# Optimization experiments

Measured on AMD Instinct MI355X. Metric: run time of the kernel, lower is better.

## Reference

```python
import jax, jax.numpy as jnp
import numpy as np

EPS = 1e-7  # K.epsilon()


def setup_inputs() -> dict:
    key = jax.random.key(0)
    k1, k2, k3 = jax.random.split(key, 3)
    B, T, D = 32, 2048, 1024
    one = jax.random.normal(k1, (B, D), dtype=jnp.float32)
    many = jax.random.normal(k2, (B, T, D), dtype=jnp.float32)
    W = jax.random.normal(k3, (D, D), dtype=jnp.float32) * (1.0 / np.sqrt(D))
    return {"one": one, "many": many, "W": W}


def reference(one, many, W):
    # logits = batch_dot(tanh(many @ W), one, axes=[2,1]) -> [B, T]
    proj = jnp.tanh(jnp.einsum('btd,de->bte', many, W))       # [B,T,D]
    logits = jnp.einsum('btd,bd->bt', proj, one)               # [B,T]
    # stable softmax with Keras epsilon in denominator
    ai = jnp.exp(logits - jnp.max(logits, axis=-1, keepdims=True))
    att_weights = ai / (jnp.sum(ai, axis=-1, keepdims=True) + EPS)  # [B,T]
    result = jnp.einsum('btd,bt->bd', many, att_weights)       # [B,D]
    return result, att_weights
```

## Files before the change

### kernel.cpp

```cpp
#include <hip/hip_runtime.h>
#include <hip/hip_bf16.h>

typedef _Float16 half8v __attribute__((ext_vector_type(8)));
typedef __fp16  fp16x2 __attribute__((ext_vector_type(2)));
typedef float floatx4 __attribute__((ext_vector_type(4)));

#define NB 32
#define NT 2048
#define ND 1024
#define NM (NB * NT)

#define GL16(g, l)                                                             \
    __builtin_amdgcn_global_load_lds(                                          \
        (const __attribute__((address_space(1))) void*)(g),                    \
        (__attribute__((address_space(3))) void*)(l), 16, 0, 0)

__device__ __forceinline__ float fast_tanh(float x) {
    x = fminf(9.0f, fmaxf(-9.0f, x));
    float e = __builtin_amdgcn_exp2f(x * 2.8853900817779268f);
    return (e - 1.0f) * __builtin_amdgcn_rcpf(e + 1.0f);
}

__global__ __launch_bounds__(256)
void wt_kernel(const float* __restrict__ W, _Float16* __restrict__ Wt) {
    __shared__ float tile[32][33];
    int tx = threadIdx.x, ty = threadIdx.y;
    int bx = blockIdx.x, by = blockIdx.y;
    #pragma unroll
    for (int i = 0; i < 4; ++i) {
        int y = by * 32 + ty + i * 8;
        tile[ty + i * 8][tx] = W[y * ND + bx * 32 + tx];
    }
    __syncthreads();
    #pragma unroll
    for (int i = 0; i < 4; ++i) {
        int e = bx * 32 + ty + i * 8;
        Wt[e * ND + by * 32 + tx] = (_Float16)tile[tx][ty + i * 8];
    }
}

__global__ __launch_bounds__(256, 2)
void gemm_logits(const float* __restrict__ many, const _Float16* __restrict__ Wt,
                 const float* __restrict__ one, float* __restrict__ logits) {
    __shared__ uint4 AsQ[2048];
    __shared__ uint4 BsQ[1024];
    char* AsB = (char*)AsQ;
    char* BsB = (char*)BsQ;

    int bid = blockIdx.x;
    int j = (bid & 7) * 512 + (bid >> 3);
    int mb = j >> 3, nb = j & 7;
    int m0 = mb * 128, n0 = nb * 128;

    int tid = threadIdx.x;
    int lane = tid & 63, w = tid >> 6;
    int wr = w >> 1, wc = w & 1;
    int l15 = lane & 15, l4 = lane >> 4;

    const char* aS = (const char*)many
        + ((size_t)(m0 + (tid >> 4)) << 12)
        + (size_t)(((tid & 15) ^ ((tid >> 4) & 7)) << 4);
    const char* bS = (const char*)Wt
        + ((size_t)(n0 + (tid >> 3)) << 11)
        + (size_t)(((tid & 7) ^ ((tid >> 3) & 7)) << 4);
    char* aD = AsB + tid * 16;
    char* bD = BsB + tid * 16;

    floatx4 acc[4][4] = {};

    for (int kb = 0; kb < 1024; kb += 64) {
        #pragma unroll
        for (int i = 0; i < 8; ++i)
            GL16(aS + kb * 4 + i * 65536, aD + i * 4096);
        #pragma unroll
        for (int i = 0; i < 4; ++i)
            GL16(bS + kb * 2 + i * 65536, bD + i * 4096);
        __syncthreads();

        #pragma unroll
        for (int ks = 0; ks < 64; ks += 32) {
            half8v af[4], bf[4];
            #pragma unroll
            for (int mi = 0; mi < 4; ++mi) {
                int r = wr * 64 + mi * 16 + l15;
                int s = l15 & 7;
                const char* base = AsB + r * 256;
                int c0 = (ks >> 2) + l4 * 2;
                float4 x = *(const float4*)(base + (size_t)((c0 ^ s) << 4));
                float4 y = *(const float4*)(base + (size_t)(((c0 + 1) ^ s) << 4));
                union { fp16x2 p[4]; half8v h; } u;
                u.p[0] = __builtin_amdgcn_cvt_pkrtz(x.x, x.y);
                u.p[1] = __builtin_amdgcn_cvt_pkrtz(x.z, x.w);
                u.p[2] = __builtin_amdgcn_cvt_pkrtz(y.x, y.y);
                u.p[3] = __builtin_amdgcn_cvt_pkrtz(y.z, y.w);
                af[mi] = u.h;
            }
            #pragma unroll
            for (int ni = 0; ni < 4; ++ni) {
                int r = wc * 64 + ni * 16 + l15;
                int s = l15 & 7;
                int c = (ks >> 3) + l4;
                bf[ni] = *(const half8v*)(BsB + r * 128 + (size_t)((c ^ s) << 4));
            }
            #pragma unroll
            for (int mi = 0; mi < 4; ++mi)
                #pragma unroll
                for (int ni = 0; ni < 4; ++ni)
                    acc[mi][ni] = __builtin_amdgcn_mfma_f32_16x16x32_f16(
                        af[mi], bf[ni], acc[mi][ni], 0, 0, 0);
        }
        __syncthreads();
    }

    int bidx = m0 >> 11;
    float onev[4];
    #pragma unroll
    for (int ni = 0; ni < 4; ++ni)
        onev[ni] = one[(bidx << 10) + n0 + wc * 64 + ni * 16 + l15];

    #pragma unroll
    for (int mi = 0; mi < 4; ++mi) {
        float part[4] = {0.f, 0.f, 0.f, 0.f};
        #pragma unroll
        for (int ni = 0; ni < 4; ++ni)
            #pragma unroll
            for (int b = 0; b < 4; ++b)
                part[b] += fast_tanh(acc[mi][ni][b]) * onev[ni];
        #pragma unroll
        for (int off = 1; off < 16; off <<= 1)
            #pragma unroll
            for (int b = 0; b < 4; ++b)
                part[b] += __shfl_xor(part[b], off, 64);
        #pragma unroll
        for (int b = 0; b < 4; ++b)
            if (l15 == mi * 4 + b)
                atomicAdd(&logits[m0 + wr * 64 + mi * 16 + l4 * 4 + b], part[b]);
    }
}

__global__ __launch_bounds__(256)
void softmax_kernel(const float* __restrict__ logits, float* __restrict__ att) {
    int b = blockIdx.x, tid = threadIdx.x;
    const float* lr = logits + (b << 11);
    float lv[8];
    float mx = -1e30f;
    #pragma unroll
    for (int i = 0; i < 8; ++i) { lv[i] = lr[tid + (i << 8)]; mx = fmaxf(mx, lv[i]); }
    #pragma unroll
    for (int off = 1; off < 64; off <<= 1) mx = fmaxf(mx, __shfl_xor(mx, off, 64));
    __shared__ float redm[4];
    __shared__ float reds[4];
    int wv = tid >> 6;
    if ((tid & 63) == 0) redm[wv] = mx;
    __syncthreads();
    mx = fmaxf(fmaxf(redm[0], redm[1]), fmaxf(redm[2], redm[3]));
    float s = 0.f;
    #pragma unroll
    for (int i = 0; i < 8; ++i) { lv[i] = expf(lv[i] - mx); s += lv[i]; }
    #pragma unroll
    for (int off = 1; off < 64; off <<= 1) s += __shfl_xor(s, off, 64);
    if ((tid & 63) == 0) reds[wv] = s;
    __syncthreads();
    s = reds[0] + reds[1] + reds[2] + reds[3];
    float inv = 1.0f / (s + 1e-7f);
    #pragma unroll
    for (int i = 0; i < 8; ++i) att[(b << 11) + tid + (i << 8)] = lv[i] * inv;
}

__global__ __launch_bounds__(256)
void out_kernel(const float* __restrict__ many, const float* __restrict__ att,
                float* __restrict__ out) {
    int b = blockIdx.x >> 4, tch = blockIdx.x & 15;
    int tid = threadIdx.x;
    __shared__ float aw[128];
    if (tid < 128) aw[tid] = att[(b << 11) + tch * 128 + tid];
    __syncthreads();
    const float* mp = many + (((size_t)b * NT + tch * 128) << 10) + tid * 4;
    float ax = 0.f, ay = 0.f, az = 0.f, aww = 0.f;
    for (int t = 0; t < 128; ++t) {
        float wgt = aw[t];
        float4 v = *reinterpret_cast<const float4*>(mp + ((size_t)t << 10));
        ax = fmaf(v.x, wgt, ax); ay = fmaf(v.y, wgt, ay);
        az = fmaf(v.z, wgt, az); aww = fmaf(v.w, wgt, aww);
    }
    float* op = out + (b << 10) + tid * 4;
    atomicAdd(op + 0, ax); atomicAdd(op + 1, ay);
    atomicAdd(op + 2, az); atomicAdd(op + 3, aww);
}

extern "C" void kernel_launch(void* const* d_in, const int* in_sizes, int n_in,
                              void* d_out, int out_size, void* d_ws, size_t ws_size,
                              hipStream_t stream) {
    const float* one  = (const float*)d_in[0];
    const float* many = (const float*)d_in[1];
    const float* W    = (const float*)d_in[2];
    float* out = (float*)d_out;

    _Float16* Wt  = (_Float16*)d_ws;
    float* logits = (float*)((char*)d_ws + (size_t)ND * ND * 2);
    float* att    = out + NB * ND;

    (void)hipMemsetAsync(out, 0, (size_t)NB * ND * sizeof(float), stream);
    (void)hipMemsetAsync(logits, 0, (size_t)NM * sizeof(float), stream);

    wt_kernel<<<dim3(32, 32), dim3(32, 8), 0, stream>>>(W, Wt);
    gemm_logits<<<4096, 256, 0, stream>>>(many, Wt, one, logits);
    softmax_kernel<<<NB, 256, 0, stream>>>(logits, att);
    out_kernel<<<NB * 16, 256, 0, stream>>>(many, att, out);
}
```

Measured before the change: 242.9 us.

## Pre-convert many to fp16 and double-buffer the GEMM LDS pipeline

After: 260.5 us. +7.2%, slower.

```diff
diff --git a/kernel.cpp b/kernel.cpp
--- a/kernel.cpp
+++ b/kernel.cpp
@@ -36,6 +36,123 @@
     for (int i = 0; i < 4; ++i) {
         int e = bx * 32 + ty + i * 8;
         Wt[e * ND + by * 32 + tx] = (_Float16)tile[tx][ty + i * 8];
+    }
+}
+
+__global__ __launch_bounds__(256)
+void conv_kernel(const float* __restrict__ many, _Float16* __restrict__ manyh) {
+    size_t idx = ((size_t)blockIdx.x * 256 + threadIdx.x) * 8;
+    size_t stride = (size_t)gridDim.x * 256 * 8;
+    for (size_t i = idx; i < (size_t)NM * ND; i += stride) {
+        float4 a = *reinterpret_cast<const float4*>(many + i);
+        float4 b = *reinterpret_cast<const float4*>(many + i + 4);
+        union { _Float16 h[8]; uint4 u; } o;
+        o.h[0] = (_Float16)a.x; o.h[1] = (_Float16)a.y;
+        o.h[2] = (_Float16)a.z; o.h[3] = (_Float16)a.w;
+        o.h[4] = (_Float16)b.x; o.h[5] = (_Float16)b.y;
+        o.h[6] = (_Float16)b.z; o.h[7] = (_Float16)b.w;
+        *reinterpret_cast<uint4*>(manyh + i) = o.u;
+    }
+}
+
+__global__ __launch_bounds__(256, 2)
+void gemm_logits_h(const _Float16* __restrict__ manyh, const _Float16* __restrict__ Wt,
+                   const float* __restrict__ one, float* __restrict__ logits) {
+    __shared__ uint4 LDSQ[4096];
+    char* Ld = (char*)LDSQ;
+
+    int bid = blockIdx.x;
+    int j = (bid & 7) * 512 + (bid >> 3);
+    int mb = j >> 3, nb = j & 7;
+    int m0 = mb * 128, n0 = nb * 128;
+
+    int tid = threadIdx.x;
+    int lane = tid & 63, w = tid >> 6;
+    int wr = w >> 1, wc = w & 1;
+    int l15 = lane & 15, l4 = lane >> 4;
+
+    const char* aS = (const char*)manyh + ((size_t)(m0 + (tid >> 3)) << 11)
+                   + (size_t)(((tid & 7) ^ ((tid >> 3) & 7)) << 4);
+    const char* bS = (const char*)Wt + ((size_t)(n0 + (tid >> 3)) << 11)
+                   + (size_t)(((tid & 7) ^ ((tid >> 3) & 7)) << 4);
+
+    floatx4 acc[4][4] = {};
+
+#define STAGE(KB, BUFOFF) do {                                                 \
+    int kby_ = (KB) * 2;                                                       \
+    _Pragma("unroll")                                                          \
+    for (int i_ = 0; i_ < 4; ++i_)                                             \
+        GL16(aS + kby_ + i_ * 65536, Ld + (BUFOFF) + tid * 16 + i_ * 4096);    \
+    _Pragma("unroll")                                                          \
+    for (int i_ = 0; i_ < 4; ++i_)                                             \
+        GL16(bS + kby_ + i_ * 65536,                                           \
+             Ld + (BUFOFF) + 16384 + tid * 16 + i_ * 4096);                    \
+} while (0)
+
+#define COMPUTE(BUFOFF) do {                                                   \
+    _Pragma("unroll")                                                          \
+    for (int ks = 0; ks < 64; ks += 32) {                                      \
+        half8v af[4], bf[4];                                                   \
+        _Pragma("unroll")                                                      \
+        for (int mi = 0; mi < 4; ++mi) {                                       \
+            int r_ = wr * 64 + mi * 16 + l15;                                  \
+            int c_ = (ks >> 3) + l4;                                           \
+            af[mi] = *(const half8v*)(Ld + (BUFOFF) + r_ * 128                 \
+                                      + ((c_ ^ (r_ & 7)) << 4));               \
+        }                                                                      \
+        _Pragma("unroll")                                                      \
+        for (int ni = 0; ni < 4; ++ni) {                                       \
+            int r_ = wc * 64 + ni * 16 + l15;                                  \
+            int c_ = (ks >> 3) + l4;                                           \
+            bf[ni] = *(const half8v*)(Ld + (BUFOFF) + 16384 + r_ * 128         \
+                                      + ((c_ ^ (r_ & 7)) << 4));               \
+        }                                                                      \
+        _Pragma("unroll")                                                      \
+        for (int mi = 0; mi < 4; ++mi)                                         \
+            _Pragma("unroll")                                                  \
+            for (int ni = 0; ni < 4; ++ni)                                     \
+                acc[mi][ni] = __builtin_amdgcn_mfma_f32_16x16x32_f16(          \
+                    af[mi], bf[ni], acc[mi][ni], 0, 0, 0);                     \
+    }                                                                          \
+} while (0)
+
+    STAGE(0, 0);
+    __syncthreads();
+    #pragma unroll 1
+    for (int t = 0; t < 16; t += 2) {
+        STAGE((t + 1) << 6, 32768);
+        COMPUTE(0);
+        __syncthreads();
+        if (t < 14) STAGE((t + 2) << 6, 0);
+        COMPUTE(32768);
+        __syncthreads();
+    }
+#undef STAGE
+#undef COMPUTE
+
+    int bidx = m0 >> 11;
+    float onev[4];
+    #pragma unroll
+    for (int ni = 0; ni < 4; ++ni)
+        onev[ni] = one[(bidx << 10) + n0 + wc * 64 + ni * 16 + l15];
+
+    #pragma unroll
+    for (int mi = 0; mi < 4; ++mi) {
+        float part[4] = {0.f, 0.f, 0.f, 0.f};
+        #pragma unroll
+        for (int ni = 0; ni < 4; ++ni)
+            #pragma unroll
+            for (int b = 0; b < 4; ++b)
+                part[b] += fast_tanh(acc[mi][ni][b]) * onev[ni];
+        #pragma unroll
+        for (int off = 1; off < 16; off <<= 1)
+            #pragma unroll
+            for (int b = 0; b < 4; ++b)
+                part[b] += __shfl_xor(part[b], off, 64);
+        #pragma unroll
+        for (int b = 0; b < 4; ++b)
+            if (l15 == mi * 4 + b)
+                atomicAdd(&logits[m0 + wr * 64 + mi * 16 + l4 * 4 + b], part[b]);
     }
 }
 
@@ -57,11 +174,9 @@
     int wr = w >> 1, wc = w & 1;
     int l15 = lane & 15, l4 = lane >> 4;
 
-    const char* aS = (const char*)many
-        + ((size_t)(m0 + (tid >> 4)) << 12)
+    const char* aS = (const char*)many + ((size_t)(m0 + (tid >> 4)) << 12)
         + (size_t)(((tid & 15) ^ ((tid >> 4) & 7)) << 4);
-    const char* bS = (const char*)Wt
-        + ((size_t)(n0 + (tid >> 3)) << 11)
+    const char* bS = (const char*)Wt + ((size_t)(n0 + (tid >> 3)) << 11)
         + (size_t)(((tid & 7) ^ ((tid >> 3) & 7)) << 4);
     char* aD = AsB + tid * 16;
     char* bD = BsB + tid * 16;
@@ -168,6 +283,28 @@
 }
 
 __global__ __launch_bounds__(256)
+void out_kernel_h(const _Float16* __restrict__ manyh, const float* __restrict__ att,
+                  float* __restrict__ out) {
+    int b = blockIdx.x >> 4, tch = blockIdx.x & 15;
+    int tid = threadIdx.x;
+    __shared__ float aw[128];
+    if (tid < 128) aw[tid] = att[(b << 11) + tch * 128 + tid];
+    __syncthreads();
+    const _Float16* mp = manyh + (((size_t)b * NT + tch * 128) << 10) + tid * 4;
+    float a0 = 0.f, a1 = 0.f, a2 = 0.f, a3 = 0.f;
+    for (int t = 0; t < 128; ++t) {
+        float wgt = aw[t];
+        union { _Float16 h[4]; uint2 u; } v;
+        v.u = *reinterpret_cast<const uint2*>(mp + ((size_t)t << 10));
+        a0 = fmaf((float)v.h[0], wgt, a0); a1 = fmaf((float)v.h[1], wgt, a1);
+        a2 = fmaf((float)v.h[2], wgt, a2); a3 = fmaf((float)v.h[3], wgt, a3);
+    }
+    float* op = out + (b << 10) + tid * 4;
+    atomicAdd(op + 0, a0); atomicAdd(op + 1, a1);
+    atomicAdd(op + 2, a2); atomicAdd(op + 3, a3);
+}
+
+__global__ __launch_bounds__(256)
 void out_kernel(const float* __restrict__ many, const float* __restrict__ att,
                 float* __restrict__ out) {
     int b = blockIdx.x >> 4, tch = blockIdx.x & 15;
@@ -196,15 +333,26 @@
     const float* W    = (const float*)d_in[2];
     float* out = (float*)d_out;
 
-    _Float16* Wt  = (_Float16*)d_ws;
-    float* logits = (float*)((char*)d_ws + (size_t)ND * ND * 2);
-    float* att    = out + NB * ND;
+    size_t wtB = (size_t)ND * ND * 2;
+    size_t lgB = (size_t)NM * 4;
+    size_t mhB = (size_t)NM * ND * 2;
+    _Float16* Wt    = (_Float16*)d_ws;
+    float*    logits = (float*)((char*)d_ws + wtB);
+    _Float16* manyh = (_Float16*)((char*)d_ws + wtB + lgB);
+    float*    att   = out + NB * ND;
+    bool big = ws_size >= wtB + lgB + mhB;
 
     (void)hipMemsetAsync(out, 0, (size_t)NB * ND * sizeof(float), stream);
     (void)hipMemsetAsync(logits, 0, (size_t)NM * sizeof(float), stream);
 
     wt_kernel<<<dim3(32, 32), dim3(32, 8), 0, stream>>>(W, Wt);
-    gemm_logits<<<4096, 256, 0, stream>>>(many, Wt, one, logits);
+    if (big) {
+        conv_kernel<<<2048, 256, 0, stream>>>(many, manyh);
+        gemm_logits_h<<<4096, 256, 0, stream>>>(manyh, Wt, one, logits);
+    } else {
+        gemm_logits<<<4096, 256, 0, stream>>>(many, Wt, one, logits);
+    }
     softmax_kernel<<<NB, 256, 0, stream>>>(logits, att);
-    out_kernel<<<NB * 16, 256, 0, stream>>>(many, att, out);
-}
+    if (big) out_kernel_h<<<NB * 16, 256, 0, stream>>>(manyh, att, out);
+    else     out_kernel<<<NB * 16, 256, 0, stream>>>(many, att, out);
+}
```
